# Kernel tuning notes

Measured on AMD Instinct MI355X. Metric: run time of the kernel, lower is better.

The kernel has to match this reference:

```python
import jax, jax.numpy as jnp
import numpy as np

C_S, C_Z, C_H = 384, 128, 32
N, L = 4, 384
EPS = 1e-5  # torch LayerNorm default


def setup_inputs() -> dict:
    key = jax.random.key(0)
    ks = jax.random.split(key, 8)
    s = jax.random.normal(ks[0], (N, L, C_S), dtype=jnp.float32)
    ln_g = jnp.ones((C_S,), jnp.float32)
    ln_b = jnp.zeros((C_S,), jnp.float32)
    W1 = jax.random.normal(ks[1], (C_S, C_H), jnp.float32) / np.sqrt(C_S)
    b1 = jax.random.normal(ks[2], (C_H,), jnp.float32) * 0.02
    W2 = jax.random.normal(ks[3], (C_S, C_H), jnp.float32) / np.sqrt(C_S)
    b2 = jax.random.normal(ks[4], (C_H,), jnp.float32) * 0.02
    # linear_out has init='final' (zeros) in training; use random values for a
    # meaningful numerical baseline.
    Wo = jax.random.normal(ks[5], (C_H * C_H, C_Z), jnp.float32) / np.sqrt(C_H * C_H)
    bo = jax.random.normal(ks[6], (C_Z,), jnp.float32) * 0.02
    return {"s": s, "ln_g": ln_g, "ln_b": ln_b, "W1": W1, "b1": b1,
            "W2": W2, "b2": b2, "Wo": Wo, "bo": bo}


def reference(s, ln_g, ln_b, W1, b1, W2, b2, Wo, bo):
    # LayerNorm over c_s
    mu = jnp.mean(s, axis=-1, keepdims=True)
    var = jnp.mean(jnp.square(s - mu), axis=-1, keepdims=True)
    sn = (s - mu) * jax.lax.rsqrt(var + EPS) * ln_g + ln_b
    a = sn @ W1 + b1  # [N, L, c_h]
    b = sn @ W2 + b2  # [N, L, c_h]
    # Original: outer product a[n,i,c]*b[n,j,d] flattened as c*c_h+d, then linear_out.
    # Algebraically fused: never materialize the [N,L,L,c_h^2] tensor.
    Wo3 = Wo.reshape(C_H, C_H, C_Z)  # index order (c, d, z) matches c*c_h+d flattening
    z = jnp.einsum('nic,njd,cdz->nijz', a, b, Wo3, optimize=True) + bo
    return z  # [N, L, L, c_z]
```

## Files before the change

### kernel.cpp

```cpp
#include <hip/hip_runtime.h>
#include <hip/hip_bf16.h>

#define CS 384
#define CH 32
#define CZ 128
#define LL 384
#define NL 1536
#define EPS 1e-5f

typedef float v2f __attribute__((ext_vector_type(2)));
typedef float v4f __attribute__((ext_vector_type(4)));
typedef short s8v __attribute__((ext_vector_type(8)));
typedef unsigned short u8s __attribute__((ext_vector_type(8)));

static __device__ __forceinline__ unsigned short f2bf(float x) {
    unsigned int b = __float_as_uint(x);
    b += 0x7FFFu + ((b >> 16) & 1u);
    return (unsigned short)(b >> 16);
}

__global__ __launch_bounds__(128) void k_ln_ab(
    const float* __restrict__ s, const float* __restrict__ g, const float* __restrict__ be,
    const float* __restrict__ W1, const float* __restrict__ b1,
    const float* __restrict__ W2, const float* __restrict__ b2,
    float* __restrict__ A, float* __restrict__ B)
{
    const int row = blockIdx.x;
    const int t   = threadIdx.x;
    const int wid = t >> 6, lane = t & 63;
    const float* srow = s + (size_t)row * CS;

    __shared__ float sn[CS];
    __shared__ float red[2];
    __shared__ float part[128];

    float x0 = srow[t], x1 = srow[t + 128], x2 = srow[t + 256];

    float p = x0 + x1 + x2;
    #pragma unroll
    for (int o = 32; o > 0; o >>= 1) p += __shfl_down(p, o);
    if (lane == 0) red[wid] = p;
    __syncthreads();
    const float mu = (red[0] + red[1]) * (1.0f / CS);
    __syncthreads();

    float d0 = x0 - mu, d1 = x1 - mu, d2 = x2 - mu;
    float q = d0 * d0 + d1 * d1 + d2 * d2;
    #pragma unroll
    for (int o = 32; o > 0; o >>= 1) q += __shfl_down(q, o);
    if (lane == 0) red[wid] = q;
    __syncthreads();
    const float var = (red[0] + red[1]) * (1.0f / CS);
    const float rstd = rsqrtf(var + EPS);

    sn[t]       = d0 * rstd * g[t]       + be[t];
    sn[t + 128] = d1 * rstd * g[t + 128] + be[t + 128];
    sn[t + 256] = d2 * rstd * g[t + 256] + be[t + 256];
    __syncthreads();

    {
        const int h    = t & 31;
        const int mat  = (t >> 5) & 1;
        const int half = t >> 6;
        const float* W = mat ? W2 : W1;
        float acc = 0.0f;
        const int c0 = half * (CS / 2);
        #pragma unroll 8
        for (int c = c0; c < c0 + CS / 2; ++c)
            acc += sn[c] * W[c * CH + h];
        part[t] = acc;
    }
    __syncthreads();
    if (t < 64) {
        const int h   = t & 31;
        const int mat = t >> 5;
        const float v = part[t] + part[t + 64] + (mat ? b2[h] : b1[h]);
        (mat ? B : A)[(size_t)row * CH + h] = v;
    }
}

__global__ __launch_bounds__(64) void k_packB(
    const float* __restrict__ B, unsigned short* __restrict__ Bf)
{
    const int jt = blockIdx.x;
    const int n  = blockIdx.y;
    const int l  = threadIdx.x;
    const int row = jt * 16 + (l & 15);
    const int g   = l >> 4;
    const float* src = B + ((size_t)(n * LL + row)) * CH + g * 8;
    u8s o;
    #pragma unroll
    for (int e = 0; e < 8; ++e) o[e] = f2bf(src[e]);
    *(u8s*)(Bf + (((size_t)(n * 24 + jt)) * 64 + l) * 8) = o;
}

__global__ __launch_bounds__(256, 2) void k_m2(
    const float* __restrict__ A, const float* __restrict__ Wo,
    unsigned short* __restrict__ Mf)
{
    const int t  = threadIdx.x;
    const int r0 = blockIdx.x * 4;
    __shared__ float Al[4][CH];
    __shared__ float Msub[4 * 32 * 128];
    if (t < 128) Al[t >> 5][t & 31] = A[(size_t)(r0 + (t >> 5)) * CH + (t & 31)];
    __syncthreads();

    const v4f* Wo4 = (const v4f*)Wo;

    #pragma unroll
    for (int it = 0; it < 4; ++it) {
        const int col = t + it * 256;
        v4f acc[4];
        #pragma unroll
        for (int r = 0; r < 4; ++r) acc[r] = (v4f)(0.f);
        #pragma unroll 8
        for (int c = 0; c < CH; ++c) {
            const v4f wv = Wo4[(size_t)c * 1024 + col];
            #pragma unroll
            for (int r = 0; r < 4; ++r)
                acc[r] += Al[r][c] * wv;
        }
        #pragma unroll
        for (int r = 0; r < 4; ++r)
            *((v4f*)&Msub[r * 4096 + col * 4]) = acc[r];
    }
    __syncthreads();

    #pragma unroll
    for (int i = 0; i < 8; ++i) {
        const int item = t + i * 256;
        const int l  = item & 63;
        const int zt = (item >> 6) & 7;
        const int rr = item >> 9;
        const int g  = l >> 4;
        const int z  = zt * 16 + (l & 15);
        u8s o;
        #pragma unroll
        for (int e = 0; e < 8; ++e)
            o[e] = f2bf(Msub[rr * 4096 + (g * 8 + e) * 128 + z]);
        *(u8s*)(Mf + (((size_t)(r0 + rr) * 8 + zt) * 64 + l) * 8) = o;
    }
}

__global__ __launch_bounds__(256, 3) void k_out(
    const unsigned short* __restrict__ Bf, const unsigned short* __restrict__ Mf,
    const float* __restrict__ bo, float* __restrict__ out)
{
    const int r = blockIdx.x;
    const int t = threadIdx.x;
    const int l = t & 63, w = t >> 6;
    const int g = l >> 4, c16 = l & 15;
    const int n = r / LL;

    s8v mf[8];
    {
        const s8v* Mfr = (const s8v*)(Mf + (size_t)r * 8 * 64 * 8);
        #pragma unroll
        for (int zt = 0; zt < 8; ++zt) mf[zt] = Mfr[zt * 64 + l];
    }
    s8v af[6];
    {
        const s8v* Bfn = (const s8v*)(Bf + (size_t)n * 24 * 64 * 8);
        #pragma unroll
        for (int i = 0; i < 6; ++i) af[i] = Bfn[(w + i * 4) * 64 + l];
    }
    v4f bov[8];
    #pragma unroll
    for (int zt = 0; zt < 8; ++zt) bov[zt] = *(const v4f*)(bo + zt * 16 + g * 4);

    v4f* outv = (v4f*)(out + (size_t)r * LL * CZ);

    #pragma unroll
    for (int i = 0; i < 6; ++i) {
        const int jt = w + i * 4;
        v4f* p = outv + (size_t)(jt * 16 + c16) * 32 + g;
        #pragma unroll
        for (int zt = 0; zt < 8; ++zt) {
            v4f d = __builtin_amdgcn_mfma_f32_16x16x32_bf16(mf[zt], af[i], (v4f)(0.f), 0, 0, 0);
            p[zt * 4] = d + bov[zt];
        }
    }
}

extern "C" void kernel_launch(void* const* d_in, const int* in_sizes, int n_in,
                              void* d_out, int out_size, void* d_ws, size_t ws_size,
                              hipStream_t stream) {
    const float* s  = (const float*)d_in[0];
    const float* g  = (const float*)d_in[1];
    const float* be = (const float*)d_in[2];
    const float* W1 = (const float*)d_in[3];
    const float* b1 = (const float*)d_in[4];
    const float* W2 = (const float*)d_in[5];
    const float* b2 = (const float*)d_in[6];
    const float* Wo = (const float*)d_in[7];
    const float* bo = (const float*)d_in[8];
    float* out = (float*)d_out;

    if (ws_size < 491520u + 12582912u) return;
    float* A  = (float*)d_ws;
    float* Bm = A + (size_t)NL * CH;
    unsigned short* Bf = (unsigned short*)((char*)d_ws + 393216);
    unsigned short* Mf = (unsigned short*)((char*)d_ws + 491520);

    k_ln_ab<<<NL, 128, 0, stream>>>(s, g, be, W1, b1, W2, b2, A, Bm);
    dim3 gpb(24, 4);
    k_packB<<<gpb, 64, 0, stream>>>(Bm, Bf);
    k_m2  <<<NL / 4, 256, 0, stream>>>(A, Wo, Mf);
    k_out <<<NL, 256, 0, stream>>>(Bf, Mf, bo, out);
}
```

Baseline: 87.86 us.

## Fuse LayerNorm, projections, B packing and M precompute into one prep kernel

Merges the LayerNorm+projection kernel, the B bf16 packing kernel, and the A·Wo precompute kernel into a single kernel of 384 blocks, each handling 4 rows. A stays in shared memory and B is written directly in the packed bf16 MFMA layout. This removes two kernel launches and the global round-trip of the fp32 A/B intermediates. In exchange, B is written with scattered 2-byte stores, and each thread walks the full 384-element dot product rather than half.

```diff
diff --git a/kernel.cpp b/kernel.cpp
--- a/kernel.cpp
+++ b/kernel.cpp
@@ -8,7 +8,6 @@
 #define NL 1536
 #define EPS 1e-5f
 
-typedef float v2f __attribute__((ext_vector_type(2)));
 typedef float v4f __attribute__((ext_vector_type(4)));
 typedef short s8v __attribute__((ext_vector_type(8)));
 typedef unsigned short u8s __attribute__((ext_vector_type(8)));
@@ -19,94 +18,66 @@
     return (unsigned short)(b >> 16);
 }
 
-__global__ __launch_bounds__(128) void k_ln_ab(
+__global__ __launch_bounds__(256, 2) void k_prep(
     const float* __restrict__ s, const float* __restrict__ g, const float* __restrict__ be,
-    const float* __restrict__ W1, const float* __restrict__ b1,
-    const float* __restrict__ W2, const float* __restrict__ b2,
-    float* __restrict__ A, float* __restrict__ B)
+    const float* __restrict__ W1, const float* __restrict__ pb1,
+    const float* __restrict__ W2, const float* __restrict__ pb2,
+    const float* __restrict__ Wo,
+    unsigned short* __restrict__ Bf, unsigned short* __restrict__ Mf)
 {
-    const int row = blockIdx.x;
+    const int blk = blockIdx.x;
+    const int r0  = blk * 4;
     const int t   = threadIdx.x;
-    const int wid = t >> 6, lane = t & 63;
-    const float* srow = s + (size_t)row * CS;
 
-    __shared__ float sn[CS];
-    __shared__ float red[2];
-    __shared__ float part[128];
+    __shared__ float sn[4][392];
+    __shared__ float Afl[4][CH];
+    __shared__ __align__(16) float Msub[4 * 32 * 128];
 
-    float x0 = srow[t], x1 = srow[t + 128], x2 = srow[t + 256];
-
-    float p = x0 + x1 + x2;
-    #pragma unroll
-    for (int o = 32; o > 0; o >>= 1) p += __shfl_down(p, o);
-    if (lane == 0) red[wid] = p;
-    __syncthreads();
-    const float mu = (red[0] + red[1]) * (1.0f / CS);
-    __syncthreads();
-
-    float d0 = x0 - mu, d1 = x1 - mu, d2 = x2 - mu;
-    float q = d0 * d0 + d1 * d1 + d2 * d2;
-    #pragma unroll
-    for (int o = 32; o > 0; o >>= 1) q += __shfl_down(q, o);
-    if (lane == 0) red[wid] = q;
-    __syncthreads();
-    const float var = (red[0] + red[1]) * (1.0f / CS);
-    const float rstd = rsqrtf(var + EPS);
-
-    sn[t]       = d0 * rstd * g[t]       + be[t];
-    sn[t + 128] = d1 * rstd * g[t + 128] + be[t + 128];
-    sn[t + 256] = d2 * rstd * g[t + 256] + be[t + 256];
+    {
+        const int w = t >> 6, lane = t & 63;
+        const float* srow = s + (size_t)(r0 + w) * CS;
+        float x[6];
+        #pragma unroll
+        for (int k = 0; k < 6; ++k) x[k] = srow[lane + k * 64];
+        float p = x[0] + x[1] + x[2] + x[3] + x[4] + x[5];
+        #pragma unroll
+        for (int m = 1; m < 64; m <<= 1) p += __shfl_xor(p, m);
+        const float mu = p * (1.0f / CS);
+        float q = 0.f;
+        #pragma unroll
+        for (int k = 0; k < 6; ++k) { float d = x[k] - mu; q += d * d; }
+        #pragma unroll
+        for (int m = 1; m < 64; m <<= 1) q += __shfl_xor(q, m);
+        const float rstd = rsqrtf(q * (1.0f / CS) + EPS);
+        #pragma unroll
+        for (int k = 0; k < 6; ++k) {
+            const int c = lane + k * 64;
+            sn[w][c] = (x[k] - mu) * rstd * g[c] + be[c];
+        }
+    }
     __syncthreads();
 
     {
-        const int h    = t & 31;
-        const int mat  = (t >> 5) & 1;
-        const int half = t >> 6;
+        const int h = t & 31, mat = (t >> 5) & 1, rw = t >> 6;
         const float* W = mat ? W2 : W1;
-        float acc = 0.0f;
-        const int c0 = half * (CS / 2);
+        const float* snr = sn[rw];
+        float acc = 0.f;
         #pragma unroll 8
-        for (int c = c0; c < c0 + CS / 2; ++c)
-            acc += sn[c] * W[c * CH + h];
-        part[t] = acc;
+        for (int c = 0; c < CS; ++c)
+            acc += snr[c] * W[c * CH + h];
+        acc += mat ? pb2[h] : pb1[h];
+        if (!mat) {
+            Afl[rw][h] = acc;
+        } else {
+            const int row = r0 + rw;
+            const int n = row / LL, jr = row % LL;
+            const int jt = jr >> 4, l16 = jr & 15;
+            Bf[(((size_t)(n * 24 + jt)) * 64 + l16 + 16 * (h >> 3)) * 8 + (h & 7)] = f2bf(acc);
+        }
     }
-    __syncthreads();
-    if (t < 64) {
-        const int h   = t & 31;
-        const int mat = t >> 5;
-        const float v = part[t] + part[t + 64] + (mat ? b2[h] : b1[h]);
-        (mat ? B : A)[(size_t)row * CH + h] = v;
-    }
-}
-
-__global__ __launch_bounds__(64) void k_packB(
-    const float* __restrict__ B, unsigned short* __restrict__ Bf)
-{
-    const int jt = blockIdx.x;
-    const int n  = blockIdx.y;
-    const int l  = threadIdx.x;
-    const int row = jt * 16 + (l & 15);
-    const int g   = l >> 4;
-    const float* src = B + ((size_t)(n * LL + row)) * CH + g * 8;
-    u8s o;
-    #pragma unroll
-    for (int e = 0; e < 8; ++e) o[e] = f2bf(src[e]);
-    *(u8s*)(Bf + (((size_t)(n * 24 + jt)) * 64 + l) * 8) = o;
-}
-
-__global__ __launch_bounds__(256, 2) void k_m2(
-    const float* __restrict__ A, const float* __restrict__ Wo,
-    unsigned short* __restrict__ Mf)
-{
-    const int t  = threadIdx.x;
-    const int r0 = blockIdx.x * 4;
-    __shared__ float Al[4][CH];
-    __shared__ float Msub[4 * 32 * 128];
-    if (t < 128) Al[t >> 5][t & 31] = A[(size_t)(r0 + (t >> 5)) * CH + (t & 31)];
     __syncthreads();
 
     const v4f* Wo4 = (const v4f*)Wo;
-
     #pragma unroll
     for (int it = 0; it < 4; ++it) {
         const int col = t + it * 256;
@@ -118,7 +89,7 @@
             const v4f wv = Wo4[(size_t)c * 1024 + col];
             #pragma unroll
             for (int r = 0; r < 4; ++r)
-                acc[r] += Al[r][c] * wv;
+                acc[r] += Afl[r][c] * wv;
         }
         #pragma unroll
         for (int r = 0; r < 4; ++r)
@@ -132,12 +103,12 @@
         const int l  = item & 63;
         const int zt = (item >> 6) & 7;
         const int rr = item >> 9;
-        const int g  = l >> 4;
+        const int gq = l >> 4;
         const int z  = zt * 16 + (l & 15);
         u8s o;
         #pragma unroll
         for (int e = 0; e < 8; ++e)
-            o[e] = f2bf(Msub[rr * 4096 + (g * 8 + e) * 128 + z]);
+            o[e] = f2bf(Msub[rr * 4096 + (gq * 8 + e) * 128 + z]);
         *(u8s*)(Mf + (((size_t)(r0 + rr) * 8 + zt) * 64 + l) * 8) = o;
     }
 }
@@ -196,15 +167,10 @@
     const float* bo = (const float*)d_in[8];
     float* out = (float*)d_out;
 
-    if (ws_size < 491520u + 12582912u) return;
-    float* A  = (float*)d_ws;
-    float* Bm = A + (size_t)NL * CH;
-    unsigned short* Bf = (unsigned short*)((char*)d_ws + 393216);
-    unsigned short* Mf = (unsigned short*)((char*)d_ws + 491520);
+    if (ws_size < 98304u + 12582912u) return;
+    unsigned short* Bf = (unsigned short*)d_ws;
+    unsigned short* Mf = (unsigned short*)((char*)d_ws + 98304);
 
-    k_ln_ab<<<NL, 128, 0, stream>>>(s, g, be, W1, b1, W2, b2, A, Bm);
-    dim3 gpb(24, 4);
-    k_packB<<<gpb, 64, 0, stream>>>(Bm, Bf);
-    k_m2  <<<NL / 4, 256, 0, stream>>>(A, Wo, Mf);
+    k_prep<<<NL / 4, 256, 0, stream>>>(s, g, be, W1, b1, W2, b2, Wo, Bf, Mf);
     k_out <<<NL, 256, 0, stream>>>(Bf, Mf, bo, out);
 }
```

Result: no change. 88.56 us (+0.8%).
